# Optimization experiments

Hardware: AMD Instinct MI355X
Metric: run time of the kernel (lower is better)

Reference implementation:

```python
import jax, jax.numpy as jnp
import numpy as np

N_NODES, N_EDGES, D, B, K, M = 100000, 500000, 172, 500, 10, 1000
MSG = 4 * D  # 2*memory_dim + edge_dim + time_dim = 688


def setup_inputs() -> dict:
    ks = jax.random.split(jax.random.key(0), 34)
    rn = lambda k, s, sc=0.05: jax.random.normal(k, s, jnp.float32) * sc
    ri = lambda k, s, hi: jax.random.randint(k, s, 0, hi, dtype=jnp.int32)
    ru = lambda k, s, sc=1000.0: jax.random.uniform(k, s, dtype=jnp.float32) * sc
    return {
        "node_feats": rn(ks[0], (N_NODES, D)),
        "edge_feats": rn(ks[1], (N_EDGES, D)),
        "memory": rn(ks[2], (N_NODES, D)),
        "time_w": rn(ks[3], (D,), 1.0),
        "time_b": rn(ks[4], (D,), 1.0),
        "W_ih": rn(ks[5], (3 * D, MSG)),
        "W_hh": rn(ks[6], (3 * D, D)),
        "b_ih": rn(ks[7], (3 * D,)),
        "b_hh": rn(ks[8], (3 * D,)),
        "lin1_w": rn(ks[9], (2, 3 * D, D)),
        "lin1_b": rn(ks[10], (2, D)),
        "lin2_w": rn(ks[11], (2, 3 * D, D)),
        "lin2_b": rn(ks[12], (2, D)),
        "aff_w1": rn(ks[13], (2 * D, D)),
        "aff_b1": rn(ks[14], (D,)),
        "aff_w2": rn(ks[15], (D, 1)),
        "aff_b2": rn(ks[16], (1,)),
        "dec_w": rn(ks[17], (D, D)),
        "dec_b": rn(ks[18], (D,)),
        "edge_times": ru(ks[19], (B,)),
        "nbr1_t": ru(ks[20], (3 * B, K)),
        "nbr2_t": ru(ks[21], (3 * B * K, K)),
        "msgs": rn(ks[22], (M, MSG)),
        "msg_times": ru(ks[23], (M,)),
        "src": ri(ks[24], (B,), N_NODES),
        "dst": ri(ks[25], (B,), N_NODES),
        "neg": ri(ks[26], (B,), N_NODES),
        "edge_idxs": ri(ks[27], (B,), N_EDGES),
        "nbr1_ids": ri(ks[28], (3 * B, K), N_NODES),
        "nbr1_eidx": ri(ks[29], (3 * B, K), N_EDGES),
        "nbr2_ids": ri(ks[30], (3 * B * K, K), N_NODES),
        "nbr2_eidx": ri(ks[31], (3 * B * K, K), N_EDGES),
        "msg_node_ids": jnp.arange(M, dtype=jnp.int32),  # unique nodes with pending messages
    }


def _time_enc(t, w, b):
    # TGN TimeEncode: cos(t * w + b), broadcast over last dim D
    return jnp.cos(t[..., None] * w + b)


def _gru(x, h, W_ih, W_hh, b_ih, b_hh):
    # torch.nn.GRUCell math
    gi = x @ W_ih.T + b_ih
    gh = h @ W_hh.T + b_hh
    ir, iz, ig = jnp.split(gi, 3, -1)
    hr, hz, hg = jnp.split(gh, 3, -1)
    r = jax.nn.sigmoid(ir + hr)
    z = jax.nn.sigmoid(iz + hz)
    g = jnp.tanh(ig + r * hg)
    return (1.0 - z) * g + z * h


def _agg(l, src_feat, ts, nbr_emb, nbr_t, edge_f, tw, tb, l1w, l1b, l2w, l2b):
    # GraphSumEmbedding.aggregate for layer index l (0-based = n_layer-1)
    dt = _time_enc(ts[:, None] - nbr_t, tw, tb)                 # [N,K,D]
    nf = jnp.concatenate([nbr_emb, dt, edge_f], -1)             # [N,K,3D]
    h = jax.nn.relu((nf @ l1w[l] + l1b[l]).sum(1))              # sum over K neighbors -> [N,D]
    st = _time_enc(jnp.zeros_like(ts), tw, tb)                  # time-embedding of delta 0
    s = jnp.concatenate([h, src_feat, st], -1)                  # [N,3D]
    return s @ l2w[l] + l2b[l]


def reference(node_feats, edge_feats, memory, time_w, time_b, W_ih, W_hh, b_ih, b_hh,
              lin1_w, lin1_b, lin2_w, lin2_b, aff_w1, aff_b1, aff_w2, aff_b2,
              dec_w, dec_b, edge_times, nbr1_t, nbr2_t, msgs, msg_times,
              src, dst, neg, edge_idxs, nbr1_ids, nbr1_eidx, nbr2_ids, nbr2_eidx,
              msg_node_ids):
    b, k = src.shape[0], nbr1_ids.shape[1]
    d = node_feats.shape[1]
    # 1) get_updated_memory: GRU update of nodes with aggregated-last messages, scatter into bank
    h_new = _gru(msgs, memory[msg_node_ids], W_ih, W_hh, b_ih, b_hh)
    mem = memory.at[msg_node_ids].set(h_new)
    feat0 = lambda n: mem[n] + node_feats[n]  # layer-0 embedding = memory + raw features
    # 2) two-layer graph-sum temporal embedding over concat(src,dst,neg)
    nodes = jnp.concatenate([src, dst, neg])                    # [3B]
    ts = jnp.concatenate([edge_times, edge_times, edge_times])  # [3B]
    n1 = nbr1_ids.reshape(-1)                                   # [3B*K]
    ts1 = jnp.repeat(ts, k)                                     # [3B*K]
    emb1 = _agg(0, feat0(n1), ts1, feat0(nbr2_ids), nbr2_t,
                edge_feats[nbr2_eidx], time_w, time_b, lin1_w, lin1_b, lin2_w, lin2_b)
    emb2 = _agg(1, feat0(nodes), ts, emb1.reshape(-1, k, d), nbr1_t,
                edge_feats[nbr1_eidx], time_w, time_b, lin1_w, lin1_b, lin2_w, lin2_b)
    s_emb, d_emb, g_emb = emb2[:b], emb2[b:2 * b], emb2[2 * b:]
    # 3) affinity (MergeLayer) scores + MLP decode + raw feature gather
    def merge(x1, x2):
        h = jax.nn.relu(jnp.concatenate([x1, x2], -1) @ aff_w1 + aff_b1)
        return (h @ aff_w2 + aff_b2).reshape(-1)
    pos_prob = jax.nn.sigmoid(merge(s_emb, d_emb))
    neg_prob = jax.nn.sigmoid(merge(s_emb, g_emb))
    decode = jnp.concatenate([s_emb, d_emb], 0) @ dec_w + dec_b
    raw = jnp.concatenate([node_feats[src], node_feats[dst]], 0)
    return (pos_prob, neg_prob, decode, raw)
```

## Files before the change

kernel.cpp:

```cpp
#include <hip/hip_runtime.h>

#define DD   172
#define TK   516
#define BB   500
#define KK   10
#define MM   1000
#define MSGW 688
#define NR1  1500
#define NR2  15000

__device__ __forceinline__ float sigm(float x){ return 1.f / (1.f + expf(-x)); }

__global__ void k_gru(const float* __restrict__ msgs, float* memory,
                      const float* __restrict__ W_ih, const float* __restrict__ W_hh,
                      const float* __restrict__ b_ih, const float* __restrict__ b_hh,
                      const int* __restrict__ ids){
  int t = threadIdx.x;
  int r0 = blockIdx.x * 8;
  __shared__ float x[8][MSGW];
  __shared__ float h[8][DD];
  __shared__ int   sid[8];
  if (t < 8) sid[t] = ids[r0 + t];
  for (int rr = 0; rr < 8; rr++)
    for (int c = t; c < MSGW; c += 192)
      x[rr][c] = msgs[(size_t)(r0 + rr)*MSGW + c];
  __syncthreads();
  if (t < DD)
    for (int rr = 0; rr < 8; rr++)
      h[rr][t] = memory[(size_t)sid[rr]*DD + t];
  __syncthreads();
  if (t < DD){
    float gi0[8], gi1[8], gi2[8];
    float bi0 = b_ih[t], bi1 = b_ih[DD+t], bi2 = b_ih[2*DD+t];
    #pragma unroll
    for (int rr = 0; rr < 8; rr++){ gi0[rr]=bi0; gi1[rr]=bi1; gi2[rr]=bi2; }
    const float* w0 = W_ih + (size_t)t*MSGW;
    const float* w1 = W_ih + (size_t)(DD+t)*MSGW;
    const float* w2 = W_ih + (size_t)(2*DD+t)*MSGW;
    for (int c = 0; c < MSGW; c++){
      float a0 = w0[c], a1 = w1[c], a2 = w2[c];
      #pragma unroll
      for (int rr = 0; rr < 8; rr++){
        float xv = x[rr][c];
        gi0[rr] = fmaf(xv, a0, gi0[rr]);
        gi1[rr] = fmaf(xv, a1, gi1[rr]);
        gi2[rr] = fmaf(xv, a2, gi2[rr]);
      }
    }
    float gh0[8], gh1[8], gh2[8];
    float bh0 = b_hh[t], bh1 = b_hh[DD+t], bh2 = b_hh[2*DD+t];
    #pragma unroll
    for (int rr = 0; rr < 8; rr++){ gh0[rr]=bh0; gh1[rr]=bh1; gh2[rr]=bh2; }
    const float* v0 = W_hh + (size_t)t*DD;
    const float* v1 = W_hh + (size_t)(DD+t)*DD;
    const float* v2 = W_hh + (size_t)(2*DD+t)*DD;
    for (int c = 0; c < DD; c++){
      float a0 = v0[c], a1 = v1[c], a2 = v2[c];
      #pragma unroll
      for (int rr = 0; rr < 8; rr++){
        float hv = h[rr][c];
        gh0[rr] = fmaf(hv, a0, gh0[rr]);
        gh1[rr] = fmaf(hv, a1, gh1[rr]);
        gh2[rr] = fmaf(hv, a2, gh2[rr]);
      }
    }
    #pragma unroll
    for (int rr = 0; rr < 8; rr++){
      float r = sigm(gi0[rr] + gh0[rr]);
      float z = sigm(gi1[rr] + gh1[rr]);
      float g = tanhf(gi2[rr] + r*gh2[rr]);
      float hn = (1.f - z)*g + z*h[rr][t];
      memory[(size_t)sid[rr]*DD + t] = hn;
    }
  }
}

__global__ void k_c2(const float* __restrict__ time_b, const float* __restrict__ lin2_w,
                     const float* __restrict__ lin2_b, float* __restrict__ consts){
  int l = blockIdx.x, j = threadIdx.x;
  __shared__ float cb[DD];
  if (j < DD) cb[j] = cosf(time_b[j]);
  __syncthreads();
  if (j < DD){
    float acc = lin2_b[(size_t)l*DD + j];
    const float* W = lin2_w + (size_t)l*TK*DD;
    for (int d = 0; d < DD; d++) acc = fmaf(cb[d], W[(size_t)(2*DD + d)*DD + j], acc);
    consts[l*DD + j] = acc;
  }
}

__global__ void k_hop2(const float* __restrict__ nf, const float* __restrict__ ef,
                       const float* __restrict__ mem, const float* __restrict__ tw,
                       const float* __restrict__ tb, const float* __restrict__ et,
                       const float* __restrict__ n2t, const int* __restrict__ n2i,
                       const int* __restrict__ n2e, const int* __restrict__ n1i,
                       const float* __restrict__ l1w, const float* __restrict__ l2w,
                       const float* __restrict__ l1b, const float* __restrict__ consts,
                       float* __restrict__ emb1){
  int t = threadIdx.x;
  int r0 = blockIdx.x * 8;
  __shared__ float S[8][TK];
  __shared__ float H[8][2*DD];
  if (t < DD){
    float w = tw[t], b = tb[t];
    for (int rr = 0; rr < 8; rr++){
      int r = r0 + rr;
      float ts = et[(r/KK) % BB];
      float sn = 0.f, sd = 0.f, se = 0.f;
      for (int k = 0; k < KK; k++){
        int id = n2i[(size_t)r*KK + k];
        int e  = n2e[(size_t)r*KK + k];
        float dt = ts - n2t[(size_t)r*KK + k];
        sn += mem[(size_t)id*DD + t] + nf[(size_t)id*DD + t];
        sd += cosf(dt*w + b);
        se += ef[(size_t)e*DD + t];
      }
      S[rr][t] = sn; S[rr][DD + t] = sd; S[rr][2*DD + t] = se;
      int sid = n1i[r];
      H[rr][DD + t] = mem[(size_t)sid*DD + t] + nf[(size_t)sid*DD + t];
    }
  }
  __syncthreads();
  if (t < DD){
    float acc[8];
    float b10 = 10.f * l1b[t];
    #pragma unroll
    for (int rr = 0; rr < 8; rr++) acc[rr] = b10;
    for (int c = 0; c < TK; c++){
      float wv = l1w[(size_t)c*DD + t];
      #pragma unroll
      for (int rr = 0; rr < 8; rr++) acc[rr] = fmaf(S[rr][c], wv, acc[rr]);
    }
    #pragma unroll
    for (int rr = 0; rr < 8; rr++) H[rr][t] = fmaxf(acc[rr], 0.f);
  }
  __syncthreads();
  if (t < DD){
    float acc[8];
    float c2 = consts[t];
    #pragma unroll
    for (int rr = 0; rr < 8; rr++) acc[rr] = c2;
    for (int c = 0; c < 2*DD; c++){
      float wv = l2w[(size_t)c*DD + t];
      #pragma unroll
      for (int rr = 0; rr < 8; rr++) acc[rr] = fmaf(H[rr][c], wv, acc[rr]);
    }
    #pragma unroll
    for (int rr = 0; rr < 8; rr++) emb1[(size_t)(r0+rr)*DD + t] = acc[rr];
  }
}

__global__ void k_hop1(const float* __restrict__ nf, const float* __restrict__ ef,
                       const float* __restrict__ mem, const float* __restrict__ tw,
                       const float* __restrict__ tb, const float* __restrict__ et,
                       const float* __restrict__ n1t, const int* __restrict__ n1e,
                       const int* __restrict__ src, const int* __restrict__ dst,
                       const int* __restrict__ neg, const float* __restrict__ emb1,
                       const float* __restrict__ l1w, const float* __restrict__ l2w,
                       const float* __restrict__ l1b, const float* __restrict__ consts,
                       float* __restrict__ emb2){
  int t = threadIdx.x;
  int r0 = blockIdx.x * 8;
  __shared__ float S[8][TK];
  __shared__ float H[8][2*DD];
  if (t < DD){
    float w = tw[t], b = tb[t];
    for (int rr = 0; rr < 8; rr++){
      int q = r0 + rr; if (q >= NR1) q = NR1 - 1;
      float ts = et[q % BB];
      float sn = 0.f, sd = 0.f, se = 0.f;
      for (int k = 0; k < KK; k++){
        int e = n1e[(size_t)q*KK + k];
        float dt = ts - n1t[(size_t)q*KK + k];
        sn += emb1[((size_t)q*KK + k)*DD + t];
        sd += cosf(dt*w + b);
        se += ef[(size_t)e*DD + t];
      }
      S[rr][t] = sn; S[rr][DD + t] = sd; S[rr][2*DD + t] = se;
      int sid = (q < BB) ? src[q] : (q < 2*BB ? dst[q - BB] : neg[q - 2*BB]);
      H[rr][DD + t] = mem[(size_t)sid*DD + t] + nf[(size_t)sid*DD + t];
    }
  }
  __syncthreads();
  if (t < DD){
    float acc[8];
    float b10 = 10.f * l1b[t];
    #pragma unroll
    for (int rr = 0; rr < 8; rr++) acc[rr] = b10;
    for (int c = 0; c < TK; c++){
      float wv = l1w[(size_t)c*DD + t];
      #pragma unroll
      for (int rr = 0; rr < 8; rr++) acc[rr] = fmaf(S[rr][c], wv, acc[rr]);
    }
    #pragma unroll
    for (int rr = 0; rr < 8; rr++) H[rr][t] = fmaxf(acc[rr], 0.f);
  }
  __syncthreads();
  if (t < DD){
    float acc[8];
    float c2 = consts[DD + t];
    #pragma unroll
    for (int rr = 0; rr < 8; rr++) acc[rr] = c2;
    for (int c = 0; c < 2*DD; c++){
      float wv = l2w[(size_t)c*DD + t];
      #pragma unroll
      for (int rr = 0; rr < 8; rr++) acc[rr] = fmaf(H[rr][c], wv, acc[rr]);
    }
    #pragma unroll
    for (int rr = 0; rr < 8; rr++){
      int q = r0 + rr;
      if (q < NR1) emb2[(size_t)q*DD + t] = acc[rr];
    }
  }
}

__global__ void k_merge(const float* __restrict__ emb2, const float* __restrict__ aff_w1,
                        const float* __restrict__ aff_b1, const float* __restrict__ aff_w2,
                        const float* __restrict__ aff_b2, float* __restrict__ out){
  int idx = blockIdx.x;
  int which = idx / BB, r = idx % BB;
  int t = threadIdx.x;
  __shared__ float x1[DD], x2[DD], hs[DD];
  if (t < DD){
    x1[t] = emb2[(size_t)r*DD + t];
    x2[t] = emb2[(size_t)(which == 0 ? BB + r : 2*BB + r)*DD + t];
  }
  __syncthreads();
  if (t < DD){
    float acc = aff_b1[t];
    for (int c = 0; c < DD; c++) acc = fmaf(x1[c], aff_w1[(size_t)c*DD + t], acc);
    for (int c = 0; c < DD; c++) acc = fmaf(x2[c], aff_w1[(size_t)(DD + c)*DD + t], acc);
    hs[t] = fmaxf(acc, 0.f) * aff_w2[t];
  }
  __syncthreads();
  if (t == 0){
    float s = aff_b2[0];
    for (int i = 0; i < DD; i++) s += hs[i];
    out[which*BB + r] = sigm(s);
  }
}

__global__ void k_dec(const float* __restrict__ emb2, const float* __restrict__ dec_w,
                      const float* __restrict__ dec_b, float* __restrict__ out){
  int t = threadIdx.x;
  int r0 = blockIdx.x * 8;
  if (t < DD){
    float acc[8];
    float bj = dec_b[t];
    #pragma unroll
    for (int rr = 0; rr < 8; rr++) acc[rr] = bj;
    for (int c = 0; c < DD; c++){
      float wv = dec_w[(size_t)c*DD + t];
      #pragma unroll
      for (int rr = 0; rr < 8; rr++)
        acc[rr] = fmaf(emb2[(size_t)(r0+rr)*DD + c], wv, acc[rr]);
    }
    #pragma unroll
    for (int rr = 0; rr < 8; rr++) out[(size_t)(r0+rr)*DD + t] = acc[rr];
  }
}

__global__ void k_raw(const float* __restrict__ node_feats, const int* __restrict__ src,
                      const int* __restrict__ dst, float* __restrict__ out){
  int q = blockIdx.x, t = threadIdx.x;
  int id = (q < BB) ? src[q] : dst[q - BB];
  if (t < DD) out[(size_t)q*DD + t] = node_feats[(size_t)id*DD + t];
}

extern "C" void kernel_launch(void* const* d_in, const int* in_sizes, int n_in,
                              void* d_out, int out_size, void* d_ws, size_t ws_size,
                              hipStream_t stream){
  (void)in_sizes; (void)n_in; (void)out_size; (void)ws_size;
  const float* node_feats = (const float*)d_in[0];
  const float* edge_feats = (const float*)d_in[1];
  float*       memory     = (float*)d_in[2];
  const float* time_w     = (const float*)d_in[3];
  const float* time_b     = (const float*)d_in[4];
  const float* W_ih       = (const float*)d_in[5];
  const float* W_hh       = (const float*)d_in[6];
  const float* b_ih       = (const float*)d_in[7];
  const float* b_hh       = (const float*)d_in[8];
  const float* lin1_w     = (const float*)d_in[9];
  const float* lin1_b     = (const float*)d_in[10];
  const float* lin2_w     = (const float*)d_in[11];
  const float* lin2_b     = (const float*)d_in[12];
  const float* aff_w1     = (const float*)d_in[13];
  const float* aff_b1     = (const float*)d_in[14];
  const float* aff_w2     = (const float*)d_in[15];
  const float* aff_b2     = (const float*)d_in[16];
  const float* dec_w      = (const float*)d_in[17];
  const float* dec_b      = (const float*)d_in[18];
  const float* edge_times = (const float*)d_in[19];
  const float* nbr1_t     = (const float*)d_in[20];
  const float* nbr2_t     = (const float*)d_in[21];
  const float* msgs       = (const float*)d_in[22];
  const int* src        = (const int*)d_in[24];
  const int* dst        = (const int*)d_in[25];
  const int* neg        = (const int*)d_in[26];
  const int* nbr1_ids   = (const int*)d_in[28];
  const int* nbr1_eidx  = (const int*)d_in[29];
  const int* nbr2_ids   = (const int*)d_in[30];
  const int* nbr2_eidx  = (const int*)d_in[31];
  const int* msg_ids    = (const int*)d_in[32];
  float* out = (float*)d_out;

  float* consts = (float*)d_ws;
  float* emb1   = (float*)((char*)d_ws + 2048);
  float* emb2   = emb1 + (size_t)NR2*DD;

  k_gru <<<MM/8, 192, 0, stream>>>(msgs, memory, W_ih, W_hh, b_ih, b_hh, msg_ids);
  k_c2  <<<2, 192, 0, stream>>>(time_b, lin2_w, lin2_b, consts);
  k_hop2<<<NR2/8, 192, 0, stream>>>(node_feats, edge_feats, memory, time_w, time_b,
                                    edge_times, nbr2_t, nbr2_ids, nbr2_eidx, nbr1_ids,
                                    lin1_w, lin2_w, lin1_b, consts, emb1);
  k_hop1<<<(NR1+7)/8, 192, 0, stream>>>(node_feats, edge_feats, memory, time_w, time_b,
                                        edge_times, nbr1_t, nbr1_eidx, src, dst, neg,
                                        emb1, lin1_w + (size_t)TK*DD, lin2_w + (size_t)TK*DD,
                                        lin1_b + DD, consts, emb2);
  k_merge<<<2*BB, 192, 0, stream>>>(emb2, aff_w1, aff_b1, aff_w2, aff_b2, out);
  k_dec <<<MM/8, 192, 0, stream>>>(emb2, dec_w, dec_b, out + 2*BB);
  k_raw <<<MM, 192, 0, stream>>>(node_feats, src, dst, out + 2*BB + (size_t)MM*DD);
}
```

Baseline: 1.102 ms.

## Transpose GRU weights, transpose smem tiles for vector reads, stage neighbor indices

```diff
diff --git a/kernel.cpp b/kernel.cpp
--- a/kernel.cpp
+++ b/kernel.cpp
@@ -11,66 +11,77 @@
 
 __device__ __forceinline__ float sigm(float x){ return 1.f / (1.f + expf(-x)); }
 
-__global__ void k_gru(const float* __restrict__ msgs, float* memory,
-                      const float* __restrict__ W_ih, const float* __restrict__ W_hh,
-                      const float* __restrict__ b_ih, const float* __restrict__ b_hh,
-                      const int* __restrict__ ids){
-  int t = threadIdx.x;
-  int r0 = blockIdx.x * 8;
-  __shared__ float x[8][MSGW];
-  __shared__ float h[8][DD];
-  __shared__ int   sid[8];
-  if (t < 8) sid[t] = ids[r0 + t];
-  for (int rr = 0; rr < 8; rr++)
-    for (int c = t; c < MSGW; c += 192)
-      x[rr][c] = msgs[(size_t)(r0 + rr)*MSGW + c];
-  __syncthreads();
-  if (t < DD)
-    for (int rr = 0; rr < 8; rr++)
-      h[rr][t] = memory[(size_t)sid[rr]*DD + t];
-  __syncthreads();
-  if (t < DD){
-    float gi0[8], gi1[8], gi2[8];
-    float bi0 = b_ih[t], bi1 = b_ih[DD+t], bi2 = b_ih[2*DD+t];
-    #pragma unroll
-    for (int rr = 0; rr < 8; rr++){ gi0[rr]=bi0; gi1[rr]=bi1; gi2[rr]=bi2; }
-    const float* w0 = W_ih + (size_t)t*MSGW;
-    const float* w1 = W_ih + (size_t)(DD+t)*MSGW;
-    const float* w2 = W_ih + (size_t)(2*DD+t)*MSGW;
+__global__ void k_tr(const float* __restrict__ in, float* __restrict__ out,
+                     int R, int C){
+  __shared__ float tile[32][33];
+  int c0 = blockIdx.x * 32, r0 = blockIdx.y * 32;
+  int tx = threadIdx.x, ty = threadIdx.y;
+  for (int i = ty; i < 32; i += 8){
+    int r = r0 + i, c = c0 + tx;
+    if (r < R && c < C) tile[i][tx] = in[(size_t)r*C + c];
+  }
+  __syncthreads();
+  for (int i = ty; i < 32; i += 8){
+    int c = c0 + i, r = r0 + tx;
+    if (c < C && r < R) out[(size_t)c*R + r] = tile[tx][i];
+  }
+}
+
+__global__ void k_gru2(const float* __restrict__ msgs, float* memory,
+                       const float* __restrict__ WT_ih,
+                       const float* __restrict__ WT_hh,
+                       const float* __restrict__ b_ih, const float* __restrict__ b_hh,
+                       const int* __restrict__ ids){
+  int t = threadIdx.x;
+  int r0 = blockIdx.x * 2;
+  __shared__ __align__(16) float xT[MSGW][2];
+  __shared__ __align__(16) float hT[DD][2];
+  int s0 = ids[r0], s1 = ids[r0 + 1];
+  for (int c = t; c < MSGW; c += 192){
+    xT[c][0] = msgs[(size_t)r0*MSGW + c];
+    xT[c][1] = msgs[(size_t)(r0+1)*MSGW + c];
+  }
+  if (t < DD){
+    hT[t][0] = memory[(size_t)s0*DD + t];
+    hT[t][1] = memory[(size_t)s1*DD + t];
+  }
+  __syncthreads();
+  if (t < DD){
+    float gi00 = b_ih[t],      gi01 = gi00;
+    float gi10 = b_ih[DD+t],   gi11 = gi10;
+    float gi20 = b_ih[2*DD+t], gi21 = gi20;
+    #pragma unroll 4
     for (int c = 0; c < MSGW; c++){
-      float a0 = w0[c], a1 = w1[c], a2 = w2[c];
-      #pragma unroll
-      for (int rr = 0; rr < 8; rr++){
-        float xv = x[rr][c];
-        gi0[rr] = fmaf(xv, a0, gi0[rr]);
-        gi1[rr] = fmaf(xv, a1, gi1[rr]);
-        gi2[rr] = fmaf(xv, a2, gi2[rr]);
-      }
-    }
-    float gh0[8], gh1[8], gh2[8];
-    float bh0 = b_hh[t], bh1 = b_hh[DD+t], bh2 = b_hh[2*DD+t];
-    #pragma unroll
-    for (int rr = 0; rr < 8; rr++){ gh0[rr]=bh0; gh1[rr]=bh1; gh2[rr]=bh2; }
-    const float* v0 = W_hh + (size_t)t*DD;
-    const float* v1 = W_hh + (size_t)(DD+t)*DD;
-    const float* v2 = W_hh + (size_t)(2*DD+t)*DD;
+      const float* wr = WT_ih + (size_t)c*TK;
+      float w0 = wr[t], w1 = wr[DD+t], w2 = wr[2*DD+t];
+      float2 xv = *reinterpret_cast<const float2*>(&xT[c][0]);
+      gi00 = fmaf(xv.x, w0, gi00); gi01 = fmaf(xv.y, w0, gi01);
+      gi10 = fmaf(xv.x, w1, gi10); gi11 = fmaf(xv.y, w1, gi11);
+      gi20 = fmaf(xv.x, w2, gi20); gi21 = fmaf(xv.y, w2, gi21);
+    }
+    float gh00 = b_hh[t],      gh01 = gh00;
+    float gh10 = b_hh[DD+t],   gh11 = gh10;
+    float gh20 = b_hh[2*DD+t], gh21 = gh20;
+    #pragma unroll 4
     for (int c = 0; c < DD; c++){
-      float a0 = v0[c], a1 = v1[c], a2 = v2[c];
-      #pragma unroll
-      for (int rr = 0; rr < 8; rr++){
-        float hv = h[rr][c];
-        gh0[rr] = fmaf(hv, a0, gh0[rr]);
-        gh1[rr] = fmaf(hv, a1, gh1[rr]);
-        gh2[rr] = fmaf(hv, a2, gh2[rr]);
-      }
-    }
-    #pragma unroll
-    for (int rr = 0; rr < 8; rr++){
-      float r = sigm(gi0[rr] + gh0[rr]);
-      float z = sigm(gi1[rr] + gh1[rr]);
-      float g = tanhf(gi2[rr] + r*gh2[rr]);
-      float hn = (1.f - z)*g + z*h[rr][t];
-      memory[(size_t)sid[rr]*DD + t] = hn;
+      const float* wr = WT_hh + (size_t)c*TK;
+      float w0 = wr[t], w1 = wr[DD+t], w2 = wr[2*DD+t];
+      float2 hv = *reinterpret_cast<const float2*>(&hT[c][0]);
+      gh00 = fmaf(hv.x, w0, gh00); gh01 = fmaf(hv.y, w0, gh01);
+      gh10 = fmaf(hv.x, w1, gh10); gh11 = fmaf(hv.y, w1, gh11);
+      gh20 = fmaf(hv.x, w2, gh20); gh21 = fmaf(hv.y, w2, gh21);
+    }
+    {
+      float r_ = sigm(gi00 + gh00);
+      float z  = sigm(gi10 + gh10);
+      float g  = tanhf(gi20 + r_*gh20);
+      memory[(size_t)s0*DD + t] = (1.f - z)*g + z*hT[t][0];
+    }
+    {
+      float r_ = sigm(gi01 + gh01);
+      float z  = sigm(gi11 + gh11);
+      float g  = tanhf(gi21 + r_*gh21);
+      memory[(size_t)s1*DD + t] = (1.f - z)*g + z*hT[t][1];
     }
   }
 }
@@ -99,25 +110,36 @@
                        float* __restrict__ emb1){
   int t = threadIdx.x;
   int r0 = blockIdx.x * 8;
-  __shared__ float S[8][TK];
-  __shared__ float H[8][2*DD];
+  __shared__ __align__(16) float S[TK][8];
+  __shared__ __align__(16) float H[2*DD][8];
+  __shared__ int   I2[8*KK], E2[8*KK], SID[8];
+  __shared__ float T2[8*KK];
+  if (t < 8*KK){
+    int r = r0 + t/KK, k = t % KK;
+    I2[t] = n2i[(size_t)r*KK + k];
+    E2[t] = n2e[(size_t)r*KK + k];
+    T2[t] = n2t[(size_t)r*KK + k];
+  }
+  if (t >= 96 && t < 104) SID[t-96] = n1i[r0 + (t-96)];
+  __syncthreads();
   if (t < DD){
     float w = tw[t], b = tb[t];
     for (int rr = 0; rr < 8; rr++){
       int r = r0 + rr;
       float ts = et[(r/KK) % BB];
       float sn = 0.f, sd = 0.f, se = 0.f;
+      #pragma unroll
       for (int k = 0; k < KK; k++){
-        int id = n2i[(size_t)r*KK + k];
-        int e  = n2e[(size_t)r*KK + k];
-        float dt = ts - n2t[(size_t)r*KK + k];
+        int id = I2[rr*KK + k];
+        int e  = E2[rr*KK + k];
+        float dt = ts - T2[rr*KK + k];
         sn += mem[(size_t)id*DD + t] + nf[(size_t)id*DD + t];
         sd += cosf(dt*w + b);
         se += ef[(size_t)e*DD + t];
       }
-      S[rr][t] = sn; S[rr][DD + t] = sd; S[rr][2*DD + t] = se;
-      int sid = n1i[r];
-      H[rr][DD + t] = mem[(size_t)sid*DD + t] + nf[(size_t)sid*DD + t];
+      S[t][rr] = sn; S[DD + t][rr] = sd; S[2*DD + t][rr] = se;
+      int sid = SID[rr];
+      H[DD + t][rr] = mem[(size_t)sid*DD + t] + nf[(size_t)sid*DD + t];
     }
   }
   __syncthreads();
@@ -126,13 +148,19 @@
     float b10 = 10.f * l1b[t];
     #pragma unroll
     for (int rr = 0; rr < 8; rr++) acc[rr] = b10;
+    const float* Wp = l1w + t;
+    #pragma unroll 4
     for (int c = 0; c < TK; c++){
-      float wv = l1w[(size_t)c*DD + t];
-      #pragma unroll
-      for (int rr = 0; rr < 8; rr++) acc[rr] = fmaf(S[rr][c], wv, acc[rr]);
-    }
-    #pragma unroll
-    for (int rr = 0; rr < 8; rr++) H[rr][t] = fmaxf(acc[rr], 0.f);
+      float wv = Wp[(size_t)c*DD];
+      float4 a = *reinterpret_cast<const float4*>(&S[c][0]);
+      float4 q = *reinterpret_cast<const float4*>(&S[c][4]);
+      acc[0] = fmaf(a.x, wv, acc[0]); acc[1] = fmaf(a.y, wv, acc[1]);
+      acc[2] = fmaf(a.z, wv, acc[2]); acc[3] = fmaf(a.w, wv, acc[3]);
+      acc[4] = fmaf(q.x, wv, acc[4]); acc[5] = fmaf(q.y, wv, acc[5]);
+      acc[6] = fmaf(q.z, wv, acc[6]); acc[7] = fmaf(q.w, wv, acc[7]);
+    }
+    #pragma unroll
+    for (int rr = 0; rr < 8; rr++) H[t][rr] = fmaxf(acc[rr], 0.f);
   }
   __syncthreads();
   if (t < DD){
@@ -140,10 +168,16 @@
     float c2 = consts[t];
     #pragma unroll
     for (int rr = 0; rr < 8; rr++) acc[rr] = c2;
+    const float* Wp = l2w + t;
+    #pragma unroll 4
     for (int c = 0; c < 2*DD; c++){
-      float wv = l2w[(size_t)c*DD + t];
-      #pragma unroll
-      for (int rr = 0; rr < 8; rr++) acc[rr] = fmaf(H[rr][c], wv, acc[rr]);
+      float wv = Wp[(size_t)c*DD];
+      float4 a = *reinterpret_cast<const float4*>(&H[c][0]);
+      float4 q = *reinterpret_cast<const float4*>(&H[c][4]);
+      acc[0] = fmaf(a.x, wv, acc[0]); acc[1] = fmaf(a.y, wv, acc[1]);
+      acc[2] = fmaf(a.z, wv, acc[2]); acc[3] = fmaf(a.w, wv, acc[3]);
+      acc[4] = fmaf(q.x, wv, acc[4]); acc[5] = fmaf(q.y, wv, acc[5]);
+      acc[6] = fmaf(q.z, wv, acc[6]); acc[7] = fmaf(q.w, wv, acc[7]);
     }
     #pragma unroll
     for (int rr = 0; rr < 8; rr++) emb1[(size_t)(r0+rr)*DD + t] = acc[rr];
@@ -161,24 +195,38 @@
                        float* __restrict__ emb2){
   int t = threadIdx.x;
   int r0 = blockIdx.x * 8;
-  __shared__ float S[8][TK];
-  __shared__ float H[8][2*DD];
+  __shared__ __align__(16) float S[TK][8];
+  __shared__ __align__(16) float H[2*DD][8];
+  __shared__ int   E1[8*KK], SID[8];
+  __shared__ float T1[8*KK];
+  if (t < 8*KK){
+    int q = r0 + t/KK; if (q >= NR1) q = NR1 - 1;
+    int k = t % KK;
+    E1[t] = n1e[(size_t)q*KK + k];
+    T1[t] = n1t[(size_t)q*KK + k];
+  }
+  if (t >= 96 && t < 104){
+    int q = r0 + (t - 96); if (q >= NR1) q = NR1 - 1;
+    SID[t-96] = (q < BB) ? src[q] : (q < 2*BB ? dst[q - BB] : neg[q - 2*BB]);
+  }
+  __syncthreads();
   if (t < DD){
     float w = tw[t], b = tb[t];
     for (int rr = 0; rr < 8; rr++){
       int q = r0 + rr; if (q >= NR1) q = NR1 - 1;
       float ts = et[q % BB];
       float sn = 0.f, sd = 0.f, se = 0.f;
+      #pragma unroll
       for (int k = 0; k < KK; k++){
-        int e = n1e[(size_t)q*KK + k];
-        float dt = ts - n1t[(size_t)q*KK + k];
+        int e = E1[rr*KK + k];
+        float dt = ts - T1[rr*KK + k];
         sn += emb1[((size_t)q*KK + k)*DD + t];
         sd += cosf(dt*w + b);
         se += ef[(size_t)e*DD + t];
       }
-      S[rr][t] = sn; S[rr][DD + t] = sd; S[rr][2*DD + t] = se;
-      int sid = (q < BB) ? src[q] : (q < 2*BB ? dst[q - BB] : neg[q - 2*BB]);
-      H[rr][DD + t] = mem[(size_t)sid*DD + t] + nf[(size_t)sid*DD + t];
+      S[t][rr] = sn; S[DD + t][rr] = sd; S[2*DD + t][rr] = se;
+      int sid = SID[rr];
+      H[DD + t][rr] = mem[(size_t)sid*DD + t] + nf[(size_t)sid*DD + t];
     }
   }
   __syncthreads();
@@ -187,13 +235,19 @@
     float b10 = 10.f * l1b[t];
     #pragma unroll
     for (int rr = 0; rr < 8; rr++) acc[rr] = b10;
+    const float* Wp = l1w + t;
+    #pragma unroll 4
     for (int c = 0; c < TK; c++){
-      float wv = l1w[(size_t)c*DD + t];
-      #pragma unroll
-      for (int rr = 0; rr < 8; rr++) acc[rr] = fmaf(S[rr][c], wv, acc[rr]);
-    }
-    #pragma unroll
-    for (int rr = 0; rr < 8; rr++) H[rr][t] = fmaxf(acc[rr], 0.f);
+      float wv = Wp[(size_t)c*DD];
+      float4 a = *reinterpret_cast<const float4*>(&S[c][0]);
+      float4 q = *reinterpret_cast<const float4*>(&S[c][4]);
+      acc[0] = fmaf(a.x, wv, acc[0]); acc[1] = fmaf(a.y, wv, acc[1]);
+      acc[2] = fmaf(a.z, wv, acc[2]); acc[3] = fmaf(a.w, wv, acc[3]);
+      acc[4] = fmaf(q.x, wv, acc[4]); acc[5] = fmaf(q.y, wv, acc[5]);
+      acc[6] = fmaf(q.z, wv, acc[6]); acc[7] = fmaf(q.w, wv, acc[7]);
+    }
+    #pragma unroll
+    for (int rr = 0; rr < 8; rr++) H[t][rr] = fmaxf(acc[rr], 0.f);
   }
   __syncthreads();
   if (t < DD){
@@ -201,10 +255,16 @@
     float c2 = consts[DD + t];
     #pragma unroll
     for (int rr = 0; rr < 8; rr++) acc[rr] = c2;
+    const float* Wp = l2w + t;
+    #pragma unroll 4
     for (int c = 0; c < 2*DD; c++){
-      float wv = l2w[(size_t)c*DD + t];
-      #pragma unroll
-      for (int rr = 0; rr < 8; rr++) acc[rr] = fmaf(H[rr][c], wv, acc[rr]);
+      float wv = Wp[(size_t)c*DD];
+      float4 a = *reinterpret_cast<const float4*>(&H[c][0]);
+      float4 q = *reinterpret_cast<const float4*>(&H[c][4]);
+      acc[0] = fmaf(a.x, wv, acc[0]); acc[1] = fmaf(a.y, wv, acc[1]);
+      acc[2] = fmaf(a.z, wv, acc[2]); acc[3] = fmaf(a.w, wv, acc[3]);
+      acc[4] = fmaf(q.x, wv, acc[4]); acc[5] = fmaf(q.y, wv, acc[5]);
+      acc[6] = fmaf(q.z, wv, acc[6]); acc[7] = fmaf(q.w, wv, acc[7]);
     }
     #pragma unroll
     for (int rr = 0; rr < 8; rr++){
@@ -233,10 +293,12 @@
     hs[t] = fmaxf(acc, 0.f) * aff_w2[t];
   }
   __syncthreads();
-  if (t == 0){
-    float s = aff_b2[0];
-    for (int i = 0; i < DD; i++) s += hs[i];
-    out[which*BB + r] = sigm(s);
+  if (t < 64){
+    float s = hs[t] + hs[t + 64];
+    if (t < DD - 128) s += hs[t + 128];
+    #pragma unroll
+    for (int off = 32; off > 0; off >>= 1) s += __shfl_down(s, off, 64);
+    if (t == 0) out[which*BB + r] = sigm(s + aff_b2[0]);
   }
 }
 
@@ -307,8 +369,12 @@
   float* consts = (float*)d_ws;
   float* emb1   = (float*)((char*)d_ws + 2048);
   float* emb2   = emb1 + (size_t)NR2*DD;
-
-  k_gru <<<MM/8, 192, 0, stream>>>(msgs, memory, W_ih, W_hh, b_ih, b_hh, msg_ids);
+  float* WT_ih  = emb1;
+  float* WT_hh  = WT_ih + (size_t)MSGW*TK;
+
+  k_tr  <<<dim3((MSGW+31)/32, (TK+31)/32), dim3(32,8), 0, stream>>>(W_ih, WT_ih, TK, MSGW);
+  k_tr  <<<dim3((DD+31)/32,   (TK+31)/32), dim3(32,8), 0, stream>>>(W_hh, WT_hh, TK, DD);
+  k_gru2<<<MM/2, 192, 0, stream>>>(msgs, memory, WT_ih, WT_hh, b_ih, b_hh, msg_ids);
   k_c2  <<<2, 192, 0, stream>>>(time_b, lin2_w, lin2_b, consts);
   k_hop2<<<NR2/8, 192, 0, stream>>>(node_feats, edge_feats, memory, time_w, time_b,
                                     edge_times, nbr2_t, nbr2_ids, nbr2_eidx, nbr1_ids,
```

New measurement: 993.7 us. -9.8%, faster.
